# Performance work log

Hardware: AMD Instinct MI355X
Metric: run time of the kernel (lower is better)

The kernel has to match this reference:

```python
import jax, jax.numpy as jnp
import numpy as np

E = 512
H = 8
D = E // H  # head_dim = 64
SCALE = D ** -0.5
NEG_INF = float('-inf')


def layer_norm(x, g, b, eps=1e-5):
    mu = jnp.mean(x, axis=-1, keepdims=True)
    var = jnp.var(x, axis=-1, keepdims=True)
    return (x - mu) * jax.lax.rsqrt(var + eps) * g + b


def setup_inputs() -> dict:
    key = jax.random.key(0)
    ks = jax.random.split(key, 16)
    B, Q, K = 4, 2048, 2048
    inp = {
        'query': jax.random.normal(ks[0], (B, Q, E), jnp.float32),
        'key_value': jax.random.normal(ks[1], (B, K, E), jnp.float32),
        'kv_mask': jax.random.randint(ks[2], (B, K), 0, 2) > 0,
        'sparse_mask': jax.random.randint(ks[3], (B, Q, K), 0, 2) > 0,
        'ln_q_g': jnp.ones((E,), jnp.float32),
        'ln_q_b': jnp.zeros((E,), jnp.float32),
        'ln_kv_g': jnp.ones((E,), jnp.float32),
        'ln_kv_b': jnp.zeros((E,), jnp.float32),
        # Linear weights stored as (in, out): y = x @ W + b
        'Wq': jax.random.normal(ks[4], (E, E), jnp.float32) * (E ** -0.5),
        'bq': jnp.zeros((E,), jnp.float32),
        'Wk': jax.random.normal(ks[5], (E, E), jnp.float32) * (E ** -0.5),
        'bk': jnp.zeros((E,), jnp.float32),
        'Wv': jax.random.normal(ks[6], (E, E), jnp.float32) * (E ** -0.5),
        'bv': jnp.zeros((E,), jnp.float32),
        'Wo': jax.random.normal(ks[7], (E, E), jnp.float32) * (E ** -0.5),
        'bo': jnp.zeros((E,), jnp.float32),
    }
    return inp


def reference(query, key_value, kv_mask, sparse_mask,
              ln_q_g, ln_q_b, ln_kv_g, ln_kv_b,
              Wq, bq, Wk, bk, Wv, bv, Wo, bo):
    B, Qn, _ = query.shape
    Kn = key_value.shape[1]
    qn = layer_norm(query, ln_q_g, ln_q_b)
    kvn = layer_norm(key_value, ln_kv_g, ln_kv_b)
    q = (qn @ Wq + bq).reshape(B, Qn, H, D)
    k = (kvn @ Wk + bk).reshape(B, Kn, H, D)
    v = (kvn @ Wv + bv).reshape(B, Kn, H, D)
    # scores: [B, H, Q, K]
    scores = jnp.einsum('bqhd,bkhd->bhqk', q, k) * SCALE
    mask = kv_mask[:, None, None, :] & sparse_mask[:, None, :, :]
    scores = jnp.where(mask, scores, NEG_INF)
    attn = jax.nn.softmax(scores, axis=-1)
    # nan_to_num(0): rows with no valid key -> all-zero weights
    valid_row = jnp.any(mask, axis=-1, keepdims=True)
    attn = jnp.where(valid_row, attn, 0.0)
    out = jnp.einsum('bhqk,bkhd->bqhd', attn, v).reshape(B, Qn, E)
    return out @ Wo + bo
```

## Files before the change

kernel.cpp:

```cpp
#include <hip/hip_runtime.h>
#include <hip/hip_bf16.h>
#include <math.h>

typedef unsigned short ushort_t;
typedef __attribute__((ext_vector_type(8))) __bf16 bf16x8;
typedef __attribute__((ext_vector_type(4))) float f32x4;
typedef __attribute__((ext_vector_type(16))) float f32x16;
typedef __attribute__((ext_vector_type(4))) unsigned int u32x4;

#define E_DIM 512
#define HEADS 8
#define HD 64
#define SEQ 2048
#define NROWS 8192
#define NEGF (-1e30f)
#define QSCALE 0.18033688011112042f

static __device__ __forceinline__ unsigned short f2b(float f) {
  unsigned int x;
  __builtin_memcpy(&x, &f, 4);
  x += 0x7fffu + ((x >> 16) & 1u);
  return (unsigned short)(x >> 16);
}

static __device__ __forceinline__ unsigned cvt_pk_bf16(float lo, float hi) {
  unsigned r;
  asm("v_cvt_pk_bf16_f32 %0, %1, %2" : "=v"(r) : "v"(lo), "v"(hi));
  return r;
}

static __device__ __forceinline__ float fexp2(float x) {
  float r;
  asm("v_exp_f32 %0, %1" : "=v"(r) : "v"(x));
  return r;
}

static __device__ __forceinline__ int swz(int row, int col) {
  return row * 64 + ((((col >> 3) ^ (row & 7)) & 7) << 3) + (col & 7);
}

static __device__ __forceinline__ void gl2lds16(const ushort_t* g, ushort_t* s) {
#if __has_builtin(__builtin_amdgcn_global_load_lds)
  __builtin_amdgcn_global_load_lds(
      (const __attribute__((address_space(1))) unsigned int*)(uintptr_t)g,
      (__attribute__((address_space(3))) unsigned int*)(uintptr_t)s,
      16, 0, 0);
#else
  int l = threadIdx.x & 63;
  *(u32x4*)(s + l * 8) = *(const u32x4*)g;
#endif
}

__launch_bounds__(256)
__global__ void prep_kernel(const float* __restrict__ Wq, const float* __restrict__ Wk,
                            const float* __restrict__ Wv, const float* __restrict__ Wo,
                            ushort_t* __restrict__ WT,
                            const int* __restrict__ kvm, const int* __restrict__ sp,
                            unsigned long long* __restrict__ bits,
                            const float* __restrict__ xq, const float* __restrict__ xkv,
                            const float* __restrict__ gq, const float* __restrict__ bq,
                            const float* __restrict__ gkv, const float* __restrict__ bkv,
                            ushort_t* __restrict__ yq, ushort_t* __restrict__ ykv) {
  int blk = blockIdx.x;
  int t = threadIdx.x;
  if (blk < 1024) {
    int z = blk >> 8, rem = blk & 255;
    const float* in = (z == 0) ? Wq : (z == 1) ? Wk : (z == 2) ? Wv : Wo;
    ushort_t* o = WT + (size_t)z * E_DIM * E_DIM;
    __shared__ float tile[32 * 33];
    int tx = t & 31, ty = t >> 5;
    int n0 = (rem & 15) * 32, k0 = (rem >> 4) * 32;
#pragma unroll
    for (int i = 0; i < 4; ++i) {
      int k = ty + i * 8;
      tile[k * 33 + tx] = in[(k0 + k) * E_DIM + n0 + tx];
    }
    __syncthreads();
#pragma unroll
    for (int i = 0; i < 4; ++i) {
      int n = ty + i * 8;
      o[(n0 + n) * E_DIM + k0 + tx] = f2b(tile[tx * 33 + n]);
    }
  } else if (blk < 3072) {
    int w = t >> 6, l = t & 63;
    int row = (blk - 1024) * 4 + w;
    int b = row >> 11;
    const int* sprow = sp + ((size_t)row << 11);
    const int* kvrow = kvm + (b << 11);
    unsigned long long* out = bits + ((size_t)row << 5);
#pragma unroll 4
    for (int it = 0; it < 32; ++it) {
      int k = it * 64 + l;
      unsigned long long m = __ballot(sprow[k] != 0 && kvrow[k] != 0);
      if (l == 0) out[it] = m;
    }
  } else {
    int idx = blk - 3072;
    int which = idx >> 11;
    const float* x = which ? xkv : xq;
    const float* g = which ? gkv : gq;
    const float* bb = which ? bkv : bq;
    ushort_t* y = which ? ykv : yq;
    int w = t >> 6, l = t & 63;
    int row = (idx & 2047) * 4 + w;
    f32x4 x0 = *(const f32x4*)&x[row * E_DIM + l * 8];
    f32x4 x1 = *(const f32x4*)&x[row * E_DIM + l * 8 + 4];
    float xf[8], s = 0.f, ss = 0.f;
#pragma unroll
    for (int j = 0; j < 8; ++j) {
      xf[j] = (j < 4) ? x0[j] : x1[j - 4];
      s += xf[j];
      ss += xf[j] * xf[j];
    }
#pragma unroll
    for (int off = 32; off > 0; off >>= 1) {
      s += __shfl_xor(s, off);
      ss += __shfl_xor(ss, off);
    }
    float mu = s * (1.f / 512.f);
    float var = fmaxf(ss * (1.f / 512.f) - mu * mu, 0.f);
    float rs = rsqrtf(var + 1e-5f);
    f32x4 g0 = *(const f32x4*)&g[l * 8];
    f32x4 g1 = *(const f32x4*)&g[l * 8 + 4];
    f32x4 b0 = *(const f32x4*)&bb[l * 8];
    f32x4 b1 = *(const f32x4*)&bb[l * 8 + 4];
#pragma unroll
    for (int j = 0; j < 8; ++j) {
      float gv = (j < 4) ? g0[j] : g1[j - 4];
      float bv = (j < 4) ? b0[j] : b1[j - 4];
      y[row * E_DIM + l * 8 + j] = f2b((xf[j] - mu) * rs * gv + bv);
    }
  }
}

template <int MODE>
static __device__ __forceinline__ void gemm_core64(ushort_t* lA, ushort_t* lB,
                                                   const ushort_t* __restrict__ A,
                                                   const ushort_t* __restrict__ WT,
                                                   const float* __restrict__ bias,
                                                   void* Cv, float scale, int m0, int n0) {
  int t = threadIdx.x, w = t >> 6, l = t & 63;
  int quad = l >> 4, l15 = l & 15;
  int wm_ = w >> 1, wn_ = w & 1;
  int csrc = ((l & 7) ^ (l >> 3)) * 8;
  int rln = l >> 3;

  f32x4 acc[4][2] = {};
  for (int kk = 0; kk < E_DIM; kk += 64) {
    __syncthreads();
#pragma unroll
    for (int i = 0; i < 4; ++i) {
      int r0 = i * 32 + w * 8;
      gl2lds16(&A[(size_t)(m0 + r0 + rln) * E_DIM + kk + csrc], &lA[r0 * 64]);
    }
#pragma unroll
    for (int i = 0; i < 2; ++i) {
      int r0 = i * 32 + w * 8;
      gl2lds16(&WT[(size_t)(n0 + r0 + rln) * E_DIM + kk + csrc], &lB[r0 * 64]);
    }
    __syncthreads();
#pragma unroll
    for (int ks = 0; ks < 2; ++ks) {
      bf16x8 af[4], bf[2];
#pragma unroll
      for (int mt = 0; mt < 4; ++mt)
        af[mt] = *(const bf16x8*)&lA[swz(wm_ * 64 + mt * 16 + l15, ks * 32 + quad * 8)];
#pragma unroll
      for (int nt = 0; nt < 2; ++nt)
        bf[nt] = *(const bf16x8*)&lB[swz(wn_ * 32 + nt * 16 + l15, ks * 32 + quad * 8)];
#pragma unroll
      for (int mt = 0; mt < 4; ++mt)
#pragma unroll
        for (int nt = 0; nt < 2; ++nt)
          acc[mt][nt] = __builtin_amdgcn_mfma_f32_16x16x32_bf16(af[mt], bf[nt], acc[mt][nt], 0, 0, 0);
    }
  }

#pragma unroll
  for (int nt = 0; nt < 2; ++nt) {
    int col = n0 + wn_ * 32 + nt * 16 + l15;
    float bv = bias[col];
    if constexpr (MODE == 2) {
      int h = col >> 6, d = col & 63;
#pragma unroll
      for (int mt = 0; mt < 4; ++mt) {
        int row = m0 + wm_ * 64 + mt * 16 + quad * 4;
        int b = row >> 11, k = row & 2047;
        union { ushort_t u[4]; uint2 v; } pk;
#pragma unroll
        for (int r = 0; r < 4; ++r) pk.u[r] = f2b(acc[mt][nt][r] + bv);
        *(uint2*)&((ushort_t*)Cv)[((((size_t)(b * HEADS + h)) * HD + d) << 11) + k] = pk.v;
      }
    } else {
#pragma unroll
      for (int mt = 0; mt < 4; ++mt) {
#pragma unroll
        for (int r = 0; r < 4; ++r) {
          int rowm = m0 + wm_ * 64 + mt * 16 + quad * 4 + r;
          float val = (acc[mt][nt][r] + bv) * scale;
          if constexpr (MODE == 0)
            ((ushort_t*)Cv)[rowm * E_DIM + col] = f2b(val);
          else
            ((float*)Cv)[rowm * E_DIM + col] = val;
        }
      }
    }
  }
}

__launch_bounds__(256)
__global__ void proj3_kernel(const ushort_t* __restrict__ qn, const ushort_t* __restrict__ WTq,
                             const float* __restrict__ bq, ushort_t* __restrict__ qp,
                             const ushort_t* __restrict__ kvn, const ushort_t* __restrict__ WTv,
                             const float* __restrict__ bv, ushort_t* __restrict__ Vt,
                             const ushort_t* __restrict__ WTk, const float* __restrict__ bk,
                             ushort_t* __restrict__ kp, int zbase) {
  __shared__ ushort_t lA[128 * 64];
  __shared__ ushort_t lB[64 * 64];
  int flat = blockIdx.x;
  int chunk = gridDim.x >> 3;
  int work = (flat & 7) * chunk + (flat >> 3);
  int z = zbase + (work >> 9);
  int r = work & 511;
  int m0 = (r >> 3) * 128, n0 = (r & 7) * 64;
  if (z == 0)      gemm_core64<0>(lA, lB, qn,  WTq, bq, qp, QSCALE, m0, n0);
  else if (z == 1) gemm_core64<2>(lA, lB, kvn, WTv, bv, Vt, 1.f,    m0, n0);
  else             gemm_core64<0>(lA, lB, kvn, WTk, bk, kp, 1.f,    m0, n0);
}

__launch_bounds__(256)
__global__ void out_kernel(const ushort_t* __restrict__ A, const ushort_t* __restrict__ WT,
                           const float* __restrict__ bias, float* __restrict__ C) {
  __shared__ ushort_t lA[128 * 64];
  __shared__ ushort_t lB[64 * 64];
  int flat = blockIdx.x;
  int work = (flat & 7) * 64 + (flat >> 3);
  int m0 = (work >> 3) * 128, n0 = (work & 7) * 64;
  gemm_core64<1>(lA, lB, A, WT, bias, C, 1.f, m0, n0);
}

__launch_bounds__(256)
__global__ void attn_kernel(const ushort_t* __restrict__ Qp, const ushort_t* __restrict__ Kp,
                            const ushort_t* __restrict__ Vt,
                            const unsigned long long* __restrict__ bits,
                            ushort_t* __restrict__ ctx) {
  __shared__ __align__(16) char smemb[40960];
  ushort_t* sQ = (ushort_t*)smemb;
  int t = threadIdx.x, w = t >> 6, l = t & 63;
  int qw = w & 1, ks = w >> 1;
  ushort_t* sK = (ushort_t*)(smemb + 8192 + ks * 8192);
  ushort_t* sV = (ushort_t*)(smemb + 24576 + ks * 8192);
  int l31 = l & 31, half = l >> 5;

  int flat = blockIdx.x;
  int work = (flat & 7) * 128 + (flat >> 3);
  int qblk = work & 31;
  int h = (work >> 5) & 7;
  int b = work >> 8;
  int q0 = qblk * 64;
  int bh = b * HEADS + h;
  int myq = qw * 32 + l31;
  int csrc = ((l & 7) ^ (l >> 3)) * 8;
  int rln = l >> 3;

#pragma unroll
  for (int it = 0; it < 2; ++it) {
    int r0 = w * 16 + it * 8;
    gl2lds16(&Qp[(size_t)(b * SEQ + q0 + r0 + rln) * E_DIM + h * HD + csrc], &sQ[r0 * 64]);
  }

  const unsigned long long* mrow = bits + ((size_t)(b * SEQ + q0 + myq) << 5);
  float ls0 = 0.f, ls1 = 0.f, ls2 = 0.f, ls3 = 0.f;
  f32x16 o0 = {}, o1 = {};
  bf16x8 qf[4];

  for (int t16 = 0; t16 < 16; ++t16) {
    int kt = t16 * 2 + ks;
    int k0 = kt * 64;
    unsigned long long wmask = mrow[kt];
    __syncthreads();
#pragma unroll
    for (int it = 0; it < 4; ++it) {
      int r0 = (it * 2 + qw) * 8;
      gl2lds16(&Kp[(size_t)(b * SEQ + k0 + r0 + rln) * E_DIM + h * HD + csrc], &sK[r0 * 64]);
      gl2lds16(&Vt[((size_t)bh * HD + r0 + rln) * SEQ + k0 + csrc], &sV[r0 * 64]);
    }
    __syncthreads();
    if (t16 == 0) {
#pragma unroll
      for (int ds = 0; ds < 4; ++ds)
        qf[ds] = *(const bf16x8*)&sQ[swz(myq, ds * 16 + 8 * half)];
    }

    f32x16 s0 = {}, s1 = {};
    __builtin_amdgcn_s_setprio(1);
#pragma unroll
    for (int ds = 0; ds < 4; ++ds) {
      bf16x8 kf0 = *(const bf16x8*)&sK[swz(l31, ds * 16 + 8 * half)];
      bf16x8 kf1 = *(const bf16x8*)&sK[swz(32 + l31, ds * 16 + 8 * half)];
      s0 = __builtin_amdgcn_mfma_f32_32x32x16_bf16(kf0, qf[ds], s0, 0, 0, 0);
      s1 = __builtin_amdgcn_mfma_f32_32x32x16_bf16(kf1, qf[ds], s1, 0, 0, 0);
    }
    __builtin_amdgcn_s_setprio(0);

    bf16x8 pf[4];
#pragma unroll
    for (int kt2 = 0; kt2 < 2; ++kt2) {
      const f32x16& sv = kt2 ? s1 : s0;
      unsigned h32 = ((unsigned)(wmask >> (32 * kt2))) >> (4 * half);
      unsigned wa[4], wb[4];
#pragma unroll
      for (int g = 0; g < 4; ++g) {
        unsigned gb = h32 >> (8 * g);
        float p0 = fexp2((gb & 1u)        ? sv[g * 4 + 0] : NEGF);
        float p1 = fexp2(((gb >> 1) & 1u) ? sv[g * 4 + 1] : NEGF);
        float p2 = fexp2(((gb >> 2) & 1u) ? sv[g * 4 + 2] : NEGF);
        float p3 = fexp2(((gb >> 3) & 1u) ? sv[g * 4 + 3] : NEGF);
        ls0 += p0; ls1 += p1; ls2 += p2; ls3 += p3;
        wa[g] = cvt_pk_bf16(p0, p1);
        wb[g] = cvt_pk_bf16(p2, p3);
      }
      asm("v_permlane32_swap_b32 %0, %1" : "+v"(wa[0]), "+v"(wa[1]));
      asm("v_permlane32_swap_b32 %0, %1" : "+v"(wb[0]), "+v"(wb[1]));
      asm("v_permlane32_swap_b32 %0, %1" : "+v"(wa[2]), "+v"(wa[3]));
      asm("v_permlane32_swap_b32 %0, %1" : "+v"(wb[2]), "+v"(wb[3]));
      union { unsigned u[4]; bf16x8 v; } f0, f1;
      f0.u[0] = wa[0]; f0.u[1] = wb[0]; f0.u[2] = wa[1]; f0.u[3] = wb[1];
      f1.u[0] = wa[2]; f1.u[1] = wb[2]; f1.u[2] = wa[3]; f1.u[3] = wb[3];
      pf[kt2 * 2 + 0] = f0.v;
      pf[kt2 * 2 + 1] = f1.v;
    }

    __builtin_amdgcn_s_setprio(1);
#pragma unroll
    for (int ksp = 0; ksp < 4; ++ksp) {
      bf16x8 vf0 = *(const bf16x8*)&sV[swz(l31, ksp * 16 + 8 * half)];
      bf16x8 vf1 = *(const bf16x8*)&sV[swz(32 + l31, ksp * 16 + 8 * half)];
      o0 = __builtin_amdgcn_mfma_f32_32x32x16_bf16(vf0, pf[ksp], o0, 0, 0, 0);
      o1 = __builtin_amdgcn_mfma_f32_32x32x16_bf16(vf1, pf[ksp], o1, 0, 0, 0);
    }
    __builtin_amdgcn_s_setprio(0);
  }

  float lsum = (ls0 + ls1) + (ls2 + ls3);
  lsum += __shfl_xor(lsum, 32);

  __syncthreads();
  float* mrg = (float*)(smemb + 8192);
  if (ks == 1) {
    float* e = mrg + (qw * 64 + l) * 33;
#pragma unroll
    for (int r = 0; r < 16; ++r) e[r] = o0[r];
#pragma unroll
    for (int r = 0; r < 16; ++r) e[16 + r] = o1[r];
    e[32] = lsum;
  }
  __syncthreads();
  if (ks == 0) {
    const float* e = mrg + (qw * 64 + l) * 33;
#pragma unroll
    for (int r = 0; r < 16; ++r) o0[r] += e[r];
#pragma unroll
    for (int r = 0; r < 16; ++r) o1[r] += e[16 + r];
    lsum += e[32];
    float inv = (lsum > 0.f) ? 1.f / lsum : 0.f;
    size_t base = (size_t)(b * SEQ + q0 + myq) * E_DIM + h * HD;
#pragma unroll
    for (int dt = 0; dt < 2; ++dt) {
      const f32x16& oo = dt ? o1 : o0;
#pragma unroll
      for (int g = 0; g < 4; ++g) {
        union { ushort_t u[4]; uint2 v; } ov;
#pragma unroll
        for (int r = 0; r < 4; ++r) ov.u[r] = f2b(oo[g * 4 + r] * inv);
        *(uint2*)&ctx[base + dt * 32 + g * 8 + 4 * half] = ov.v;
      }
    }
  }
}

extern "C" void kernel_launch(void* const* d_in, const int* in_sizes, int n_in,
                              void* d_out, int out_size, void* d_ws, size_t ws_size,
                              hipStream_t stream) {
  const float* query     = (const float*)d_in[0];
  const float* key_value = (const float*)d_in[1];
  const int*   kv_mask   = (const int*)d_in[2];
  const int*   sp_mask   = (const int*)d_in[3];
  const float* ln_q_g  = (const float*)d_in[4];
  const float* ln_q_b  = (const float*)d_in[5];
  const float* ln_kv_g = (const float*)d_in[6];
  const float* ln_kv_b = (const float*)d_in[7];
  const float* Wq = (const float*)d_in[8];
  const float* bq = (const float*)d_in[9];
  const float* Wk = (const float*)d_in[10];
  const float* bk = (const float*)d_in[11];
  const float* Wv = (const float*)d_in[12];
  const float* bv = (const float*)d_in[13];
  const float* Wo = (const float*)d_in[14];
  const float* bo = (const float*)d_in[15];

  const size_t NB = (size_t)NROWS * E_DIM;
  char* ws = (char*)d_ws;
  ushort_t* bufA = (ushort_t*)ws;
  ushort_t* bufB = bufA + NB;
  ushort_t* WT   = bufB + NB;
  ushort_t* WTq = WT;
  ushort_t* WTk = WTq + E_DIM * E_DIM;
  ushort_t* WTv = WTk + E_DIM * E_DIM;
  ushort_t* WTo = WTv + E_DIM * E_DIM;
  unsigned long long* bits = (unsigned long long*)(WTo + E_DIM * E_DIM);
  ushort_t* bufC = (ushort_t*)(ws + (20u << 20));

  ushort_t* dlo = (ushort_t*)d_out;
  ushort_t* dhi = dlo + NB;

  bool fused = ws_size >= (28u << 20);
  ushort_t* kp = fused ? bufC : dlo;

  prep_kernel<<<7168, 256, 0, stream>>>(Wq, Wk, Wv, Wo, WT, kv_mask, sp_mask, bits,
                                        query, key_value, ln_q_g, ln_q_b, ln_kv_g, ln_kv_b,
                                        dlo, bufA);

  if (fused) {
    proj3_kernel<<<1536, 256, 0, stream>>>(dlo, WTq, bq, dhi,
                                           bufA, WTv, bv, bufB,
                                           WTk, bk, bufC, 0);
  } else {
    proj3_kernel<<<1024, 256, 0, stream>>>(dlo, WTq, bq, dhi,
                                           bufA, WTv, bv, bufB,
                                           WTk, bk, dlo, 0);
    proj3_kernel<<<512, 256, 0, stream>>>(dlo, WTq, bq, dhi,
                                          bufA, WTv, bv, bufB,
                                          WTk, bk, dlo, 2);
  }

  attn_kernel<<<1024, 256, 0, stream>>>(dhi, kp, bufB, bits, bufA);

  out_kernel<<<512, 256, 0, stream>>>(bufA, WTo, bo, (float*)d_out);
}
```

Before: 259.6 us.

## Load attention K/V/Q fragments directly from global memory instead of LDS staging

The attention kernel drops its LDS staging of Q, K and V tiles along with the two per-iteration block barriers. Each wave now loads its MFMA operand fragments straight from global memory (relying on L1/L2 caching) and interleaves score and PV MFMAs per 32-key half. The mask select before exp2 is replaced by an AND with a sign-extended bit mask after exp2. This removes barrier stalls and LDS traffic, but each wave issues redundant global loads, since both q-waves read the same K/V, and it loses the coalesced bulk copy into LDS.

```diff
diff --git a/kernel.cpp b/kernel.cpp
--- a/kernel.cpp
+++ b/kernel.cpp
@@ -13,7 +13,6 @@
 #define HD 64
 #define SEQ 2048
 #define NROWS 8192
-#define NEGF (-1e30f)
 #define QSCALE 0.18033688011112042f
 
 static __device__ __forceinline__ unsigned short f2b(float f) {
@@ -33,6 +32,14 @@
   float r;
   asm("v_exp_f32 %0, %1" : "=v"(r) : "v"(x));
   return r;
+}
+
+static __device__ __forceinline__ unsigned bitmask1(unsigned v, int off) {
+#if __has_builtin(__builtin_amdgcn_sbfe)
+  return (unsigned)__builtin_amdgcn_sbfe((int)v, off, 1);
+#else
+  return (unsigned)((int)(v << (31 - off)) >> 31);
+#endif
 }
 
 static __device__ __forceinline__ int swz(int row, int col) {
@@ -244,12 +251,9 @@
                             const ushort_t* __restrict__ Vt,
                             const unsigned long long* __restrict__ bits,
                             ushort_t* __restrict__ ctx) {
-  __shared__ __align__(16) char smemb[40960];
-  ushort_t* sQ = (ushort_t*)smemb;
+  __shared__ float mrg[2 * 64 * 33];
   int t = threadIdx.x, w = t >> 6, l = t & 63;
   int qw = w & 1, ks = w >> 1;
-  ushort_t* sK = (ushort_t*)(smemb + 8192 + ks * 8192);
-  ushort_t* sV = (ushort_t*)(smemb + 24576 + ks * 8192);
   int l31 = l & 31, half = l >> 5;
 
   int flat = blockIdx.x;
@@ -260,62 +264,45 @@
   int q0 = qblk * 64;
   int bh = b * HEADS + h;
   int myq = qw * 32 + l31;
-  int csrc = ((l & 7) ^ (l >> 3)) * 8;
-  int rln = l >> 3;
-
-#pragma unroll
-  for (int it = 0; it < 2; ++it) {
-    int r0 = w * 16 + it * 8;
-    gl2lds16(&Qp[(size_t)(b * SEQ + q0 + r0 + rln) * E_DIM + h * HD + csrc], &sQ[r0 * 64]);
-  }
+
+  const ushort_t* qrow = Qp + (size_t)(b * SEQ + q0 + myq) * E_DIM + h * HD;
+  bf16x8 qf[4];
+#pragma unroll
+  for (int ds = 0; ds < 4; ++ds)
+    qf[ds] = *(const bf16x8*)&qrow[ds * 16 + 8 * half];
 
   const unsigned long long* mrow = bits + ((size_t)(b * SEQ + q0 + myq) << 5);
+  const ushort_t* Kbase = Kp + (size_t)(b * SEQ) * E_DIM + h * HD;
+  const ushort_t* Vbase = Vt + (size_t)bh * HD * SEQ;
+
   float ls0 = 0.f, ls1 = 0.f, ls2 = 0.f, ls3 = 0.f;
   f32x16 o0 = {}, o1 = {};
-  bf16x8 qf[4];
 
   for (int t16 = 0; t16 < 16; ++t16) {
     int kt = t16 * 2 + ks;
     int k0 = kt * 64;
     unsigned long long wmask = mrow[kt];
-    __syncthreads();
-#pragma unroll
-    for (int it = 0; it < 4; ++it) {
-      int r0 = (it * 2 + qw) * 8;
-      gl2lds16(&Kp[(size_t)(b * SEQ + k0 + r0 + rln) * E_DIM + h * HD + csrc], &sK[r0 * 64]);
-      gl2lds16(&Vt[((size_t)bh * HD + r0 + rln) * SEQ + k0 + csrc], &sV[r0 * 64]);
-    }
-    __syncthreads();
-    if (t16 == 0) {
-#pragma unroll
-      for (int ds = 0; ds < 4; ++ds)
-        qf[ds] = *(const bf16x8*)&sQ[swz(myq, ds * 16 + 8 * half)];
-    }
-
-    f32x16 s0 = {}, s1 = {};
-    __builtin_amdgcn_s_setprio(1);
-#pragma unroll
-    for (int ds = 0; ds < 4; ++ds) {
-      bf16x8 kf0 = *(const bf16x8*)&sK[swz(l31, ds * 16 + 8 * half)];
-      bf16x8 kf1 = *(const bf16x8*)&sK[swz(32 + l31, ds * 16 + 8 * half)];
-      s0 = __builtin_amdgcn_mfma_f32_32x32x16_bf16(kf0, qf[ds], s0, 0, 0, 0);
-      s1 = __builtin_amdgcn_mfma_f32_32x32x16_bf16(kf1, qf[ds], s1, 0, 0, 0);
-    }
-    __builtin_amdgcn_s_setprio(0);
-
-    bf16x8 pf[4];
+
 #pragma unroll
     for (int kt2 = 0; kt2 < 2; ++kt2) {
-      const f32x16& sv = kt2 ? s1 : s0;
+      const ushort_t* krow = Kbase + (size_t)(k0 + 32 * kt2 + l31) * E_DIM;
+      f32x16 s = {};
+      __builtin_amdgcn_s_setprio(1);
+#pragma unroll
+      for (int ds = 0; ds < 4; ++ds) {
+        bf16x8 kf = *(const bf16x8*)&krow[ds * 16 + 8 * half];
+        s = __builtin_amdgcn_mfma_f32_32x32x16_bf16(kf, qf[ds], s, 0, 0, 0);
+      }
+      __builtin_amdgcn_s_setprio(0);
+
       unsigned h32 = ((unsigned)(wmask >> (32 * kt2))) >> (4 * half);
       unsigned wa[4], wb[4];
 #pragma unroll
       for (int g = 0; g < 4; ++g) {
-        unsigned gb = h32 >> (8 * g);
-        float p0 = fexp2((gb & 1u)        ? sv[g * 4 + 0] : NEGF);
-        float p1 = fexp2(((gb >> 1) & 1u) ? sv[g * 4 + 1] : NEGF);
-        float p2 = fexp2(((gb >> 2) & 1u) ? sv[g * 4 + 2] : NEGF);
-        float p3 = fexp2(((gb >> 3) & 1u) ? sv[g * 4 + 3] : NEGF);
+        float p0 = __uint_as_float(__float_as_uint(fexp2(s[g * 4 + 0])) & bitmask1(h32, 8 * g + 0));
+        float p1 = __uint_as_float(__float_as_uint(fexp2(s[g * 4 + 1])) & bitmask1(h32, 8 * g + 1));
+        float p2 = __uint_as_float(__float_as_uint(fexp2(s[g * 4 + 2])) & bitmask1(h32, 8 * g + 2));
+        float p3 = __uint_as_float(__float_as_uint(fexp2(s[g * 4 + 3])) & bitmask1(h32, 8 * g + 3));
         ls0 += p0; ls1 += p1; ls2 += p2; ls3 += p3;
         wa[g] = cvt_pk_bf16(p0, p1);
         wb[g] = cvt_pk_bf16(p2, p3);
@@ -327,26 +314,24 @@
       union { unsigned u[4]; bf16x8 v; } f0, f1;
       f0.u[0] = wa[0]; f0.u[1] = wb[0]; f0.u[2] = wa[1]; f0.u[3] = wb[1];
       f1.u[0] = wa[2]; f1.u[1] = wb[2]; f1.u[2] = wa[3]; f1.u[3] = wb[3];
-      pf[kt2 * 2 + 0] = f0.v;
-      pf[kt2 * 2 + 1] = f1.v;
-    }
-
-    __builtin_amdgcn_s_setprio(1);
-#pragma unroll
-    for (int ksp = 0; ksp < 4; ++ksp) {
-      bf16x8 vf0 = *(const bf16x8*)&sV[swz(l31, ksp * 16 + 8 * half)];
-      bf16x8 vf1 = *(const bf16x8*)&sV[swz(32 + l31, ksp * 16 + 8 * half)];
-      o0 = __builtin_amdgcn_mfma_f32_32x32x16_bf16(vf0, pf[ksp], o0, 0, 0, 0);
-      o1 = __builtin_amdgcn_mfma_f32_32x32x16_bf16(vf1, pf[ksp], o1, 0, 0, 0);
-    }
-    __builtin_amdgcn_s_setprio(0);
+
+      __builtin_amdgcn_s_setprio(1);
+#pragma unroll
+      for (int kl = 0; kl < 2; ++kl) {
+        int kc = (kt2 * 2 + kl) * 16 + 8 * half;
+        bf16x8 vf0 = *(const bf16x8*)&Vbase[(size_t)l31 * SEQ + k0 + kc];
+        bf16x8 vf1 = *(const bf16x8*)&Vbase[(size_t)(32 + l31) * SEQ + k0 + kc];
+        const bf16x8& pfx = kl ? f1.v : f0.v;
+        o0 = __builtin_amdgcn_mfma_f32_32x32x16_bf16(vf0, pfx, o0, 0, 0, 0);
+        o1 = __builtin_amdgcn_mfma_f32_32x32x16_bf16(vf1, pfx, o1, 0, 0, 0);
+      }
+      __builtin_amdgcn_s_setprio(0);
+    }
   }
 
   float lsum = (ls0 + ls1) + (ls2 + ls3);
   lsum += __shfl_xor(lsum, 32);
 
-  __syncthreads();
-  float* mrg = (float*)(smemb + 8192);
   if (ks == 1) {
     float* e = mrg + (qw * 64 + l) * 33;
 #pragma unroll
```

New measurement: 353.7 us. +36.3%, slower.
